# Kernel optimization log

Measured on AMD Instinct MI355X. Metric: run time of the kernel, lower is better.

The kernel has to match this reference:

```python
import jax, jax.numpy as jnp
import numpy as np

EPS = 1e-8  # F.cosine_similarity eps
K = 2       # prompt_length


def setup_inputs() -> dict:
    key = jax.random.key(0)
    k1, k2, k3, k4 = jax.random.split(key, 4)
    B, DIM, NP, D = 32, 64, 4, 1024   # P: [batch, dim, N_p, D]; D == V (rows of stored table)
    E, VC = 768, 32000                 # stored table [V=D, E]; f_e: E -> vocab_dim=VC
    P = jax.random.normal(k1, (B, DIM, NP, D), dtype=jnp.float32)
    we_stored = jax.random.normal(k2, (D, E), dtype=jnp.float32) * 0.02
    fe_w = jax.random.normal(k3, (VC, E), dtype=jnp.float32) * 0.02
    fe_b = jax.random.normal(k4, (VC,), dtype=jnp.float32) * 0.02
    return {"P": P, "we_stored": we_stored, "fe_w": fe_w, "fe_b": fe_b}


def reference(P, we_stored, fe_w, fe_b):
    # word_embeddings = f_e(stored).t()  ->  [vocab_dim, V] == [VC, D]
    T = (we_stored @ fe_w.T + fe_b).T            # [VC, D]
    B, DIM, NP, D = P.shape
    # Cosine sim of each tiled embedding row (repeated N_p times) vs flattened P_i:
    #   dot(tiled_w, P_flat) = w . sum_j P[..., j, :]
    #   ||tiled_w|| = sqrt(N_p) * ||w||
    s = P.sum(axis=2)                                             # [B, DIM, D]
    w_norm = jnp.maximum(jnp.sqrt(jnp.float32(NP)) * jnp.linalg.norm(T, axis=1), EPS)   # [VC]
    p_norm = jnp.maximum(jnp.linalg.norm(P.reshape(B, DIM, -1), axis=-1), EPS)          # [B, DIM]
    scores = jnp.einsum('bdk,vk->bdv', s, T) / (w_norm[None, None, :] * p_norm[..., None])  # [B, DIM, VC]
    values, indices = jax.lax.top_k(scores, K)                    # [B, DIM, K]
    e_k = T[indices]                                              # [B, DIM, K, D]
    Z = jnp.concatenate([e_k, P], axis=2)                         # [B, DIM, NP+K, D]
    return Z, values
```

## Files before the change

### kernel.cpp

```cpp
#include <hip/hip_runtime.h>
#include <hip/hip_bf16.h>
#include <math.h>

#define B_    32
#define DIM_  64
#define NP_   4
#define D_    1024
#define E_    768
#define VC_   32000
#define R_    2048
#define KTOP  2
#define EPS_  1e-8f
#define NCB   250
#define NCAND 8

#define T_OFF    ((size_t)0)
#define S_OFF    (T_OFF + (size_t)VC_ * D_)
#define INVW_OFF (S_OFF + (size_t)R_ * D_)
#define INVP_OFF (INVW_OFF + VC_)
#define WSQ_OFF  (INVP_OFF + R_)
#define PV_OFF   (WSQ_OFF + VC_)
#define PI_OFF   (PV_OFF + (size_t)R_ * NCB * 2)
#define SB_OFF   (PI_OFF + (size_t)R_ * NCB * 2)
#define TB_OFF   (SB_OFF + (size_t)R_ * D_ / 2)
#define WH_OFF   (TB_OFF + (size_t)VC_ * D_ / 2)
#define WL_OFF   (WH_OFF + (size_t)D_ * E_ / 2)
#define CAND_OFF (WL_OFF + (size_t)D_ * E_ / 2)
#define TIDX_OFF (CAND_OFF + (size_t)R_ * NCAND)
#define AH_OFF   (TIDX_OFF + (size_t)R_ * 2)
#define AL_OFF   (AH_OFF + (size_t)VC_ * E_ / 2)

#define NEG_INF (-3.4e38f)

typedef __bf16 bf16x8 __attribute__((ext_vector_type(8)));
typedef unsigned short u16x8 __attribute__((ext_vector_type(8)));
typedef float  f32x4  __attribute__((ext_vector_type(4)));

__device__ __forceinline__ void async_ld16(const void* gptr, void* lptr) {
    __builtin_amdgcn_global_load_lds(
        (const __attribute__((address_space(1))) void*)(uintptr_t)gptr,
        (__attribute__((address_space(3))) void*)(unsigned)(uintptr_t)lptr,
        16, 0, 0);
}

__device__ __forceinline__ bool better(float v, int i, float bv, int bi) {
    return (v > bv) || (v == bv && i < bi);
}

__global__ __launch_bounds__(256) void k_zero(float* __restrict__ wsq) {
    int i = blockIdx.x * 256 + threadIdx.x;
    if (i < VC_) wsq[i] = 0.f;
}

__global__ __launch_bounds__(256) void k_split(const float* __restrict__ x,
                                               unsigned short* __restrict__ hi,
                                               unsigned short* __restrict__ lo) {
    int i = (blockIdx.x * 256 + threadIdx.x) * 4;
    float4 v = *(const float4*)(x + i);
    ushort4 h, l;
    __bf16 b;
    b = (__bf16)v.x; h.x = __builtin_bit_cast(unsigned short, b); l.x = __builtin_bit_cast(unsigned short, (__bf16)(v.x - (float)b));
    b = (__bf16)v.y; h.y = __builtin_bit_cast(unsigned short, b); l.y = __builtin_bit_cast(unsigned short, (__bf16)(v.y - (float)b));
    b = (__bf16)v.z; h.z = __builtin_bit_cast(unsigned short, b); l.z = __builtin_bit_cast(unsigned short, (__bf16)(v.z - (float)b));
    b = (__bf16)v.w; h.w = __builtin_bit_cast(unsigned short, b); l.w = __builtin_bit_cast(unsigned short, (__bf16)(v.w - (float)b));
    *(ushort4*)(hi + i) = h;
    *(ushort4*)(lo + i) = l;
}

__global__ __launch_bounds__(256) void k_sum_pnorm(const float* __restrict__ P,
                                                   float* __restrict__ s,
                                                   unsigned short* __restrict__ sb,
                                                   float* __restrict__ invp) {
    int r = blockIdx.x;
    int t = threadIdx.x;
    const float* base = P + (size_t)r * NP_ * D_;
    float4 acc = make_float4(0.f, 0.f, 0.f, 0.f);
    float sq = 0.f;
#pragma unroll
    for (int np = 0; np < NP_; ++np) {
        float4 v = *(const float4*)(base + (size_t)np * D_ + t * 4);
        acc.x += v.x; acc.y += v.y; acc.z += v.z; acc.w += v.w;
        sq += v.x * v.x + v.y * v.y + v.z * v.z + v.w * v.w;
    }
    *(float4*)(s + (size_t)r * D_ + t * 4) = acc;
    ushort4 o;
    __bf16 b;
    b = (__bf16)acc.x; o.x = __builtin_bit_cast(unsigned short, b);
    b = (__bf16)acc.y; o.y = __builtin_bit_cast(unsigned short, b);
    b = (__bf16)acc.z; o.z = __builtin_bit_cast(unsigned short, b);
    b = (__bf16)acc.w; o.w = __builtin_bit_cast(unsigned short, b);
    *(ushort4*)(sb + (size_t)r * D_ + t * 4) = o;

    __shared__ float red[256];
    red[t] = sq;
    __syncthreads();
    for (int off = 128; off > 0; off >>= 1) {
        if (t < off) red[t] += red[t + off];
        __syncthreads();
    }
    if (t == 0) invp[r] = 1.0f / fmaxf(sqrtf(red[0]), EPS_);
}

__global__ __launch_bounds__(256) void k_gemm_T_mfma(const unsigned short* __restrict__ Ahg,
                                                     const unsigned short* __restrict__ Alg,
                                                     const unsigned short* __restrict__ Bhg,
                                                     const unsigned short* __restrict__ Blg,
                                                     const float* __restrict__ bias,
                                                     float* __restrict__ T,
                                                     unsigned short* __restrict__ Tb,
                                                     float* __restrict__ wsq) {
    __shared__ __align__(16) unsigned short Ash[2][128 * 32];
    __shared__ __align__(16) unsigned short Asl[2][128 * 32];
    __shared__ __align__(16) unsigned short Bsh[2][128 * 32];
    __shared__ __align__(16) unsigned short Bsl[2][128 * 32];

    int tid = threadIdx.x;
    int wid = tid >> 6, lane = tid & 63;
    int quad = lane >> 4, l15 = lane & 15;
    int id  = blockIdx.x;
    int swz = (id & 7) * 250 + (id >> 3);
    int v0 = (swz >> 3) * 128;
    int d0 = (swz & 7) * 128;
    int vband = (wid & 1) * 64, nband = (wid >> 1) * 64;

    f32x4 acc[4][4];
#pragma unroll
    for (int i = 0; i < 4; ++i)
#pragma unroll
        for (int j = 0; j < 4; ++j) acc[i][j] = f32x4{0.f, 0.f, 0.f, 0.f};

    int r_lane = lane >> 2;
    int slot   = lane & 3;

#define STAGE_G(buf, kk)                                                           \
    {                                                                              \
_Pragma("unroll")                                                                  \
        for (int j = 0; j < 2; ++j) {                                              \
            int rowt = wid * 32 + j * 16 + r_lane;                                 \
            int ss = (slot - (rowt >> 1)) & 3;                                     \
            void* la = (void*)(Ash[buf] + (wid * 32 + j * 16) * 32);               \
            void* lb = (void*)(Asl[buf] + (wid * 32 + j * 16) * 32);               \
            void* lc = (void*)(Bsh[buf] + (wid * 32 + j * 16) * 32);               \
            void* ld = (void*)(Bsl[buf] + (wid * 32 + j * 16) * 32);               \
            async_ld16(Ahg + (size_t)(v0 + rowt) * E_ + (kk) + ss * 8, la);        \
            async_ld16(Alg + (size_t)(v0 + rowt) * E_ + (kk) + ss * 8, lb);        \
            async_ld16(Bhg + (size_t)(d0 + rowt) * E_ + (kk) + ss * 8, lc);        \
            async_ld16(Blg + (size_t)(d0 + rowt) * E_ + (kk) + ss * 8, ld);        \
        }                                                                          \
    }

    int cur = 0;
    STAGE_G(0, 0);
    __syncthreads();

    for (int k0 = 0; k0 < E_; k0 += 32) {
        if (k0 + 32 < E_) STAGE_G(cur ^ 1, k0 + 32);

        bf16x8 fah[4], fal[4], fbh[4], fbl[4];
#pragma unroll
        for (int mt = 0; mt < 4; ++mt) {
            int row = vband + mt * 16 + l15;
            int ps = (quad + (row >> 1)) & 3;
            int off = row * 32 + ps * 8;
            fah[mt] = *(const bf16x8*)(Ash[cur] + off);
            fal[mt] = *(const bf16x8*)(Asl[cur] + off);
        }
#pragma unroll
        for (int nt = 0; nt < 4; ++nt) {
            int row = nband + nt * 16 + l15;
            int ps = (quad + (row >> 1)) & 3;
            int off = row * 32 + ps * 8;
            fbh[nt] = *(const bf16x8*)(Bsh[cur] + off);
            fbl[nt] = *(const bf16x8*)(Bsl[cur] + off);
        }
#pragma unroll
        for (int mt = 0; mt < 4; ++mt)
#pragma unroll
            for (int nt = 0; nt < 4; ++nt) {
                acc[mt][nt] = __builtin_amdgcn_mfma_f32_16x16x32_bf16(fah[mt], fbh[nt], acc[mt][nt], 0, 0, 0);
                acc[mt][nt] = __builtin_amdgcn_mfma_f32_16x16x32_bf16(fal[mt], fbh[nt], acc[mt][nt], 0, 0, 0);
                acc[mt][nt] = __builtin_amdgcn_mfma_f32_16x16x32_bf16(fah[mt], fbl[nt], acc[mt][nt], 0, 0, 0);
            }

        __syncthreads();
        cur ^= 1;
    }
#undef STAGE_G

    float sq[4][4] = {};
#pragma unroll
    for (int mt = 0; mt < 4; ++mt) {
        int vbase = v0 + vband + mt * 16 + quad * 4;
        float bv[4];
#pragma unroll
        for (int rg = 0; rg < 4; ++rg) bv[rg] = bias[vbase + rg];
#pragma unroll
        for (int nt = 0; nt < 4; ++nt) {
            int d = d0 + nband + nt * 16 + l15;
#pragma unroll
            for (int rg = 0; rg < 4; ++rg) {
                float val = acc[mt][nt][rg] + bv[rg];
                T[(size_t)(vbase + rg) * D_ + d] = val;
                __bf16 vb = (__bf16)val;
                Tb[(size_t)(vbase + rg) * D_ + d] = __builtin_bit_cast(unsigned short, vb);
                sq[mt][rg] += val * val;
            }
        }
    }
#pragma unroll
    for (int mt = 0; mt < 4; ++mt)
#pragma unroll
        for (int rg = 0; rg < 4; ++rg) {
            float p = sq[mt][rg];
            p += __shfl_xor(p, 1); p += __shfl_xor(p, 2);
            p += __shfl_xor(p, 4); p += __shfl_xor(p, 8);
            if (l15 == 0) atomicAdd(&wsq[v0 + vband + mt * 16 + quad * 4 + rg], p);
        }
}

__global__ __launch_bounds__(256) void k_invw(const float* __restrict__ wsq,
                                              float* __restrict__ invw) {
    int v = blockIdx.x * 256 + threadIdx.x;
    if (v < VC_) invw[v] = 1.0f / fmaxf(2.0f * sqrtf(wsq[v]), EPS_);
}

__global__ __launch_bounds__(512) void k_scores_mfma(const unsigned short* __restrict__ Tb,
                                                     const unsigned short* __restrict__ sb,
                                                     const float* __restrict__ invw,
                                                     float* __restrict__ pval,
                                                     int* __restrict__ pidx) {
    __shared__ __align__(16) unsigned short As[4][256 * 32];
    __shared__ __align__(16) unsigned short Bs[4][256 * 32];

    int tid = threadIdx.x;
    int wid = tid >> 6, lane = tid & 63;
    int quad = lane >> 4, l15 = lane & 15;
    int wm = wid >> 2, wn = wid & 3;
    int id   = blockIdx.x;
    int swz  = (id & 7) * 125 + (id >> 3);
    int vblk = swz >> 3;
    int rblk = swz & 7;
    int v0 = vblk * 256;
    int r0 = rblk * 256;

    f32x4 acc[8][4];
#pragma unroll
    for (int i = 0; i < 8; ++i)
#pragma unroll
        for (int j = 0; j < 4; ++j) acc[i][j] = f32x4{0.f, 0.f, 0.f, 0.f};

    int r_lane = lane >> 2;
    int slot   = lane & 3;

#define STAGE_SC(buf, kk)                                                          \
    {                                                                              \
_Pragma("unroll")                                                                  \
        for (int j = 0; j < 2; ++j) {                                              \
            int rowt = j * 128 + wid * 16 + r_lane;                                \
            int ss = (slot - (rowt >> 1)) & 3;                                     \
            async_ld16(Tb + (size_t)(v0 + rowt) * D_ + (kk) + ss * 8,              \
                       (void*)(As[buf] + (j * 128 + wid * 16) * 32));              \
            async_ld16(sb + (size_t)(r0 + rowt) * D_ + (kk) + ss * 8,              \
                       (void*)(Bs[buf] + (j * 128 + wid * 16) * 32));              \
        }                                                                          \
    }

    STAGE_SC(0, 0);
    STAGE_SC(1, 32);
    STAGE_SC(2, 64);

    const int NT = D_ / 32;
    for (int kt = 0; kt < NT; ++kt) {
        int cur = kt & 3;
        int kn  = (kt + 3 < NT) ? (kt + 3) * 32 : kt * 32;
        STAGE_SC((kt + 3) & 3, kn);

        asm volatile("s_waitcnt vmcnt(12)" ::: "memory");
        __builtin_amdgcn_s_barrier();
        asm volatile("" ::: "memory");

        bf16x8 bfr[4];
#pragma unroll
        for (int nt = 0; nt < 4; ++nt) {
            int row = wn * 64 + nt * 16 + l15;
            int ps = (quad + (row >> 1)) & 3;
            bfr[nt] = *(const bf16x8*)(Bs[cur] + row * 32 + ps * 8);
        }
        __builtin_amdgcn_s_setprio(1);
#pragma unroll
        for (int mt = 0; mt < 8; ++mt) {
            int row = wm * 128 + mt * 16 + l15;
            int ps = (quad + (row >> 1)) & 3;
            bf16x8 af = *(const bf16x8*)(As[cur] + row * 32 + ps * 8);
#pragma unroll
            for (int nt = 0; nt < 4; ++nt)
                acc[mt][nt] = __builtin_amdgcn_mfma_f32_16x16x32_bf16(af, bfr[nt], acc[mt][nt], 0, 0, 0);
        }
        __builtin_amdgcn_s_setprio(0);

        __builtin_amdgcn_sched_barrier(0);
        __builtin_amdgcn_s_barrier();
        asm volatile("" ::: "memory");
    }
#undef STAGE_SC

    float iw[8][4];
#pragma unroll
    for (int mt = 0; mt < 8; ++mt)
#pragma unroll
        for (int rg = 0; rg < 4; ++rg)
            iw[mt][rg] = invw[v0 + wm * 128 + mt * 16 + quad * 4 + rg];

#pragma unroll
    for (int nt = 0; nt < 4; ++nt) {
        float b1 = NEG_INF, b2 = NEG_INF;
        int i1 = 0x7fffffff, i2 = 0x7fffffff;
#pragma unroll
        for (int mt = 0; mt < 8; ++mt)
#pragma unroll
            for (int rg = 0; rg < 4; ++rg) {
                float val = acc[mt][nt][rg] * iw[mt][rg];
                int v = v0 + wm * 128 + mt * 16 + quad * 4 + rg;
                if (better(val, v, b1, i1)) { b2 = b1; i2 = i1; b1 = val; i1 = v; }
                else if (better(val, v, b2, i2)) { b2 = val; i2 = v; }
            }
#pragma unroll
        for (int off = 16; off <= 32; off <<= 1) {
            float o1 = __shfl_xor(b1, off), o2 = __shfl_xor(b2, off);
            int  oi1 = __shfl_xor(i1, off), oi2 = __shfl_xor(i2, off);
            if (better(o1, oi1, b1, i1)) {
                if (better(b1, i1, o2, oi2)) { b2 = b1; i2 = i1; } else { b2 = o2; i2 = oi2; }
                b1 = o1; i1 = oi1;
            } else if (better(o1, oi1, b2, i2)) { b2 = o1; i2 = oi1; }
        }
        if (quad == 0) {
            int rl = wn * 64 + nt * 16 + l15;
            size_t off = ((size_t)(r0 + rl) * NCB + vblk * 2 + wm) * 2;
            pval[off] = b1;     pidx[off] = i1;
            pval[off + 1] = b2; pidx[off + 1] = i2;
        }
    }
}

__global__ __launch_bounds__(256) void k_topk8(const float* __restrict__ pval,
                                               const int* __restrict__ pidx,
                                               int* __restrict__ cands) {
    int r = blockIdx.x, t = threadIdx.x;
    __shared__ float v[512];
    __shared__ int  id[512];
    for (int c = t; c < 512; c += 256) {
        if (c < NCB * 2) { v[c] = pval[(size_t)r * NCB * 2 + c]; id[c] = pidx[(size_t)r * NCB * 2 + c]; }
        else             { v[c] = NEG_INF; id[c] = 0x7fffffff; }
    }
    __syncthreads();
    if (t == 0) {
        float bv[NCAND]; int bi[NCAND];
#pragma unroll
        for (int j = 0; j < NCAND; ++j) { bv[j] = NEG_INF; bi[j] = 0x7fffffff; }
        for (int c = 0; c < NCB * 2; ++c) {
            float x = v[c]; int xi = id[c];
            if (better(x, xi, bv[NCAND - 1], bi[NCAND - 1])) {
                int j = NCAND - 1;
                while (j > 0 && better(x, xi, bv[j - 1], bi[j - 1])) {
                    bv[j] = bv[j - 1]; bi[j] = bi[j - 1]; --j;
                }
                bv[j] = x; bi[j] = xi;
            }
        }
#pragma unroll
        for (int j = 0; j < NCAND; ++j) cands[r * NCAND + j] = bi[j];
    }
}

__global__ __launch_bounds__(256) void k_rescore(const float* __restrict__ s,
                                                 const float* __restrict__ T,
                                                 const int* __restrict__ cands,
                                                 const float* __restrict__ invw,
                                                 const float* __restrict__ invp,
                                                 float* __restrict__ outv,
                                                 int* __restrict__ tidx) {
    int r = blockIdx.x, t = threadIdx.x;
    int cg = t >> 5, l32 = t & 31;
    int c = cands[r * NCAND + cg];
    const float* Trow = T + (size_t)c * D_;
    const float* srow = s + (size_t)r * D_;
    float p = 0.f;
#pragma unroll
    for (int j = 0; j < 8; ++j) {
        int e = (j * 32 + l32) * 4;
        float4 a = *(const float4*)(srow + e);
        float4 b = *(const float4*)(Trow + e);
        p += a.x * b.x + a.y * b.y + a.z * b.z + a.w * b.w;
    }
#pragma unroll
    for (int off = 16; off >= 1; off >>= 1) p += __shfl_xor(p, off);
    __shared__ float sc[NCAND];
    if (l32 == 0) sc[cg] = p;
    __syncthreads();
    if (t == 0) {
        float ip = invp[r];
        float b1 = NEG_INF, b2 = NEG_INF;
        int i1 = 0x7fffffff, i2 = 0x7fffffff;
#pragma unroll
        for (int j = 0; j < NCAND; ++j) {
            int ci = cands[r * NCAND + j];
            float val = sc[j] * invw[ci] * ip;
            if (better(val, ci, b1, i1)) { b2 = b1; i2 = i1; b1 = val; i1 = ci; }
            else if (better(val, ci, b2, i2)) { b2 = val; i2 = ci; }
        }
        outv[(size_t)r * 2 + 0] = b1;
        outv[(size_t)r * 2 + 1] = b2;
        tidx[r * 2 + 0] = i1;
        tidx[r * 2 + 1] = i2;
    }
}

__global__ __launch_bounds__(256) void k_writeZ(const float* __restrict__ P,
                                                const float* __restrict__ T,
                                                const int* __restrict__ tidx,
                                                float* __restrict__ out) {
    int blk = blockIdx.x;
    int r = blk / 6, j = blk - r * 6;
    const float* src;
    if (j < KTOP) src = T + (size_t)tidx[r * 2 + j] * D_;
    else          src = P + ((size_t)r * NP_ + (j - KTOP)) * D_;
    float4 v = *(const float4*)(src + threadIdx.x * 4);
    *(float4*)(out + ((size_t)r * 6 + j) * D_ + threadIdx.x * 4) = v;
}

extern "C" void kernel_launch(void* const* d_in, const int* in_sizes, int n_in,
                              void* d_out, int out_size, void* d_ws, size_t ws_size,
                              hipStream_t stream) {
    const float* P   = (const float*)d_in[0];
    const float* we  = (const float*)d_in[1];
    const float* few = (const float*)d_in[2];
    const float* feb = (const float*)d_in[3];
    float* out = (float*)d_out;
    float* ws  = (float*)d_ws;

    float* T    = ws + T_OFF;
    float* s    = ws + S_OFF;
    float* invw = ws + INVW_OFF;
    float* invp = ws + INVP_OFF;
    float* wsq  = ws + WSQ_OFF;
    float* pval = ws + PV_OFF;
    int*   pidx = (int*)(ws + PI_OFF);
    unsigned short* sb  = (unsigned short*)(ws + SB_OFF);
    unsigned short* Tb  = (unsigned short*)(ws + TB_OFF);
    unsigned short* weh = (unsigned short*)(ws + WH_OFF);
    unsigned short* wel = (unsigned short*)(ws + WL_OFF);
    int*   cands = (int*)(ws + CAND_OFF);
    int*   tidx  = (int*)(ws + TIDX_OFF);
    unsigned short* fewh = (unsigned short*)(ws + AH_OFF);
    unsigned short* fewl = (unsigned short*)(ws + AL_OFF);
    float* outv = out + (size_t)R_ * 6 * D_;

    k_zero<<<(VC_ + 255) / 256, 256, 0, stream>>>(wsq);
    k_split<<<(D_ * E_) / 1024, 256, 0, stream>>>(we, weh, wel);
    k_split<<<((size_t)VC_ * E_) / 1024, 256, 0, stream>>>(few, fewh, fewl);
    k_sum_pnorm<<<R_, 256, 0, stream>>>(P, s, sb, invp);
    k_gemm_T_mfma<<<2000, 256, 0, stream>>>(fewh, fewl, weh, wel, feb, T, Tb, wsq);
    k_invw<<<(VC_ + 255) / 256, 256, 0, stream>>>(wsq, invw);
    k_scores_mfma<<<1000, 512, 0, stream>>>(Tb, sb, invw, pval, pidx);
    k_topk8<<<R_, 256, 0, stream>>>(pval, pidx, cands);
    k_rescore<<<R_, 256, 0, stream>>>(s, T, cands, invw, invp, outv, tidx);
    k_writeZ<<<R_ * 6, 256, 0, stream>>>(P, T, tidx, out);
}
```

Baseline: 661.5 us.

## Enlarge T-GEMM tile to 256x128 with 512 threads and triple-buffered async loads

```diff
diff --git a/kernel.cpp b/kernel.cpp
--- a/kernel.cpp
+++ b/kernel.cpp
@@ -101,7 +101,7 @@
     if (t == 0) invp[r] = 1.0f / fmaxf(sqrtf(red[0]), EPS_);
 }
 
-__global__ __launch_bounds__(256) void k_gemm_T_mfma(const unsigned short* __restrict__ Ahg,
+__global__ __launch_bounds__(512) void k_gemm_T_mfma(const unsigned short* __restrict__ Ahg,
                                                      const unsigned short* __restrict__ Alg,
                                                      const unsigned short* __restrict__ Bhg,
                                                      const unsigned short* __restrict__ Blg,
@@ -109,19 +109,19 @@
                                                      float* __restrict__ T,
                                                      unsigned short* __restrict__ Tb,
                                                      float* __restrict__ wsq) {
-    __shared__ __align__(16) unsigned short Ash[2][128 * 32];
-    __shared__ __align__(16) unsigned short Asl[2][128 * 32];
-    __shared__ __align__(16) unsigned short Bsh[2][128 * 32];
-    __shared__ __align__(16) unsigned short Bsl[2][128 * 32];
+    __shared__ __align__(16) unsigned short Ash[3][256 * 32];
+    __shared__ __align__(16) unsigned short Asl[3][256 * 32];
+    __shared__ __align__(16) unsigned short Bsh[3][128 * 32];
+    __shared__ __align__(16) unsigned short Bsl[3][128 * 32];
 
     int tid = threadIdx.x;
     int wid = tid >> 6, lane = tid & 63;
     int quad = lane >> 4, l15 = lane & 15;
+    int wm = wid >> 1, wn = wid & 1;
     int id  = blockIdx.x;
-    int swz = (id & 7) * 250 + (id >> 3);
-    int v0 = (swz >> 3) * 128;
+    int swz = (id & 7) * 125 + (id >> 3);
+    int v0 = (swz >> 3) * 256;
     int d0 = (swz & 7) * 128;
-    int vband = (wid & 1) * 64, nband = (wid >> 1) * 64;
 
     f32x4 acc[4][4];
 #pragma unroll
@@ -132,71 +132,84 @@
     int r_lane = lane >> 2;
     int slot   = lane & 3;
 
-#define STAGE_G(buf, kk)                                                           \
+#define STAGE_T(buf, kk)                                                           \
     {                                                                              \
 _Pragma("unroll")                                                                  \
         for (int j = 0; j < 2; ++j) {                                              \
-            int rowt = wid * 32 + j * 16 + r_lane;                                 \
+            int rowt = j * 128 + wid * 16 + r_lane;                                \
             int ss = (slot - (rowt >> 1)) & 3;                                     \
-            void* la = (void*)(Ash[buf] + (wid * 32 + j * 16) * 32);               \
-            void* lb = (void*)(Asl[buf] + (wid * 32 + j * 16) * 32);               \
-            void* lc = (void*)(Bsh[buf] + (wid * 32 + j * 16) * 32);               \
-            void* ld = (void*)(Bsl[buf] + (wid * 32 + j * 16) * 32);               \
-            async_ld16(Ahg + (size_t)(v0 + rowt) * E_ + (kk) + ss * 8, la);        \
-            async_ld16(Alg + (size_t)(v0 + rowt) * E_ + (kk) + ss * 8, lb);        \
-            async_ld16(Bhg + (size_t)(d0 + rowt) * E_ + (kk) + ss * 8, lc);        \
-            async_ld16(Blg + (size_t)(d0 + rowt) * E_ + (kk) + ss * 8, ld);        \
+            async_ld16(Ahg + (size_t)(v0 + rowt) * E_ + (kk) + ss * 8,             \
+                       (void*)(Ash[buf] + (j * 128 + wid * 16) * 32));             \
+            async_ld16(Alg + (size_t)(v0 + rowt) * E_ + (kk) + ss * 8,             \
+                       (void*)(Asl[buf] + (j * 128 + wid * 16) * 32));             \
         }                                                                          \
-    }
-
+        {                                                                          \
+            int rowb = wid * 16 + r_lane;                                          \
+            int ssb = (slot - (rowb >> 1)) & 3;                                    \
+            async_ld16(Bhg + (size_t)(d0 + rowb) * E_ + (kk) + ssb * 8,            \
+                       (void*)(Bsh[buf] + (wid * 16) * 32));                       \
+            async_ld16(Blg + (size_t)(d0 + rowb) * E_ + (kk) + ssb * 8,            \
+                       (void*)(Bsl[buf] + (wid * 16) * 32));                       \
+        }                                                                          \
+    }
+
+    STAGE_T(0, 0);
+    STAGE_T(1, 32);
+
+    const int NT = E_ / 32;
     int cur = 0;
-    STAGE_G(0, 0);
-    __syncthreads();
-
-    for (int k0 = 0; k0 < E_; k0 += 32) {
-        if (k0 + 32 < E_) STAGE_G(cur ^ 1, k0 + 32);
-
-        bf16x8 fah[4], fal[4], fbh[4], fbl[4];
-#pragma unroll
-        for (int mt = 0; mt < 4; ++mt) {
-            int row = vband + mt * 16 + l15;
-            int ps = (quad + (row >> 1)) & 3;
-            int off = row * 32 + ps * 8;
-            fah[mt] = *(const bf16x8*)(Ash[cur] + off);
-            fal[mt] = *(const bf16x8*)(Asl[cur] + off);
-        }
+    for (int kt = 0; kt < NT; ++kt) {
+        int kn = (kt + 2 < NT) ? (kt + 2) * 32 : kt * 32;
+        int nb = cur + 2; if (nb >= 3) nb -= 3;
+        STAGE_T(nb, kn);
+
+        asm volatile("s_waitcnt vmcnt(12)" ::: "memory");
+        __builtin_amdgcn_s_barrier();
+        asm volatile("" ::: "memory");
+
+        bf16x8 fbh[4], fbl[4];
 #pragma unroll
         for (int nt = 0; nt < 4; ++nt) {
-            int row = nband + nt * 16 + l15;
+            int row = wn * 64 + nt * 16 + l15;
             int ps = (quad + (row >> 1)) & 3;
             int off = row * 32 + ps * 8;
             fbh[nt] = *(const bf16x8*)(Bsh[cur] + off);
             fbl[nt] = *(const bf16x8*)(Bsl[cur] + off);
         }
-#pragma unroll
-        for (int mt = 0; mt < 4; ++mt)
+        __builtin_amdgcn_s_setprio(1);
+#pragma unroll
+        for (int mt = 0; mt < 4; ++mt) {
+            int row = wm * 64 + mt * 16 + l15;
+            int ps = (quad + (row >> 1)) & 3;
+            int off = row * 32 + ps * 8;
+            bf16x8 fah = *(const bf16x8*)(Ash[cur] + off);
+            bf16x8 fal = *(const bf16x8*)(Asl[cur] + off);
 #pragma unroll
             for (int nt = 0; nt < 4; ++nt) {
-                acc[mt][nt] = __builtin_amdgcn_mfma_f32_16x16x32_bf16(fah[mt], fbh[nt], acc[mt][nt], 0, 0, 0);
-                acc[mt][nt] = __builtin_amdgcn_mfma_f32_16x16x32_bf16(fal[mt], fbh[nt], acc[mt][nt], 0, 0, 0);
-                acc[mt][nt] = __builtin_amdgcn_mfma_f32_16x16x32_bf16(fah[mt], fbl[nt], acc[mt][nt], 0, 0, 0);
+                acc[mt][nt] = __builtin_amdgcn_mfma_f32_16x16x32_bf16(fah, fbh[nt], acc[mt][nt], 0, 0, 0);
+                acc[mt][nt] = __builtin_amdgcn_mfma_f32_16x16x32_bf16(fal, fbh[nt], acc[mt][nt], 0, 0, 0);
+                acc[mt][nt] = __builtin_amdgcn_mfma_f32_16x16x32_bf16(fah, fbl[nt], acc[mt][nt], 0, 0, 0);
             }
-
-        __syncthreads();
-        cur ^= 1;
-    }
-#undef STAGE_G
+        }
+        __builtin_amdgcn_s_setprio(0);
+
+        __builtin_amdgcn_sched_barrier(0);
+        __builtin_amdgcn_s_barrier();
+        asm volatile("" ::: "memory");
+        cur = (cur == 2) ? 0 : cur + 1;
+    }
+#undef STAGE_T
 
     float sq[4][4] = {};
 #pragma unroll
     for (int mt = 0; mt < 4; ++mt) {
-        int vbase = v0 + vband + mt * 16 + quad * 4;
+        int vbase = v0 + wm * 64 + mt * 16 + quad * 4;
         float bv[4];
 #pragma unroll
         for (int rg = 0; rg < 4; ++rg) bv[rg] = bias[vbase + rg];
 #pragma unroll
         for (int nt = 0; nt < 4; ++nt) {
-            int d = d0 + nband + nt * 16 + l15;
+            int d = d0 + wn * 64 + nt * 16 + l15;
 #pragma unroll
             for (int rg = 0; rg < 4; ++rg) {
                 float val = acc[mt][nt][rg] + bv[rg];
@@ -214,7 +227,7 @@
             float p = sq[mt][rg];
             p += __shfl_xor(p, 1); p += __shfl_xor(p, 2);
             p += __shfl_xor(p, 4); p += __shfl_xor(p, 8);
-            if (l15 == 0) atomicAdd(&wsq[v0 + vband + mt * 16 + quad * 4 + rg], p);
+            if (l15 == 0) atomicAdd(&wsq[v0 + wm * 64 + mt * 16 + quad * 4 + rg], p);
         }
 }
 
@@ -459,7 +472,7 @@
     k_split<<<(D_ * E_) / 1024, 256, 0, stream>>>(we, weh, wel);
     k_split<<<((size_t)VC_ * E_) / 1024, 256, 0, stream>>>(few, fewh, fewl);
     k_sum_pnorm<<<R_, 256, 0, stream>>>(P, s, sb, invp);
-    k_gemm_T_mfma<<<2000, 256, 0, stream>>>(fewh, fewl, weh, wel, feb, T, Tb, wsq);
+    k_gemm_T_mfma<<<1000, 512, 0, stream>>>(fewh, fewl, weh, wel, feb, T, Tb, wsq);
     k_invw<<<(VC_ + 255) / 256, 256, 0, stream>>>(wsq, invw);
     k_scores_mfma<<<1000, 512, 0, stream>>>(Tb, sb, invw, pval, pidx);
     k_topk8<<<R_, 256, 0, stream>>>(pval, pidx, cands);
```

Measured after the change: 676.8 us. 1.02x slower.
